# Kernel optimization log

Measured on AMD Instinct MI355X. Metric: run time of the kernel, lower is better.

Reference implementation:

```python
import jax, jax.numpy as jnp
import numpy as np
import math

N_NODES = 2000
LOOKBACK = 24
IN_DIM = 16
EMB_DIM = 64
BATCH = 32
LN_EPS = 1e-5


def _layernorm(v, g, b):
    mu = jnp.mean(v, axis=-1, keepdims=True)
    var = jnp.var(v, axis=-1, keepdims=True)
    return (v - mu) * jax.lax.rsqrt(var + LN_EPS) * g + b


def setup_inputs() -> dict:
    key = jax.random.key(0)
    ks = jax.random.split(key, 12)
    td = LOOKBACK * IN_DIM  # 384
    s_in = 1.0 / math.sqrt(td)
    s_d = 1.0 / math.sqrt(IN_DIM)
    return {
        "x": jax.random.normal(ks[0], (BATCH, N_NODES, LOOKBACK, IN_DIM), jnp.float32),
        "Wq": jax.random.normal(ks[1], (td, EMB_DIM), jnp.float32) * s_in,
        "bq": jax.random.normal(ks[2], (EMB_DIM,), jnp.float32) * 0.01,
        "Wk": jax.random.normal(ks[3], (td, EMB_DIM), jnp.float32) * s_in,
        "bk": jax.random.normal(ks[4], (EMB_DIM,), jnp.float32) * 0.01,
        "g0": jnp.ones((EMB_DIM,), jnp.float32),
        "beta0": jnp.zeros((EMB_DIM,), jnp.float32),
        "g1": jnp.ones((EMB_DIM,), jnp.float32),
        "beta1": jnp.zeros((EMB_DIM,), jnp.float32),
        "normal": jax.random.normal(ks[5], (N_NODES, LOOKBACK, IN_DIM), jnp.float32),
        "Win": jax.random.normal(ks[6], (IN_DIM, IN_DIM), jnp.float32) * s_d,
    }


def reference(x, Wq, bq, Wk, bk, g0, beta0, g1, beta1, normal, Win):
    b, n, t, d = x.shape
    xf = x.reshape(b, n, t * d)
    # per-sample q/k linear + layernorm (batched over b)
    q1 = _layernorm(xf @ Wq + bq, g0, beta0)  # (b, n, e)
    k1 = _layernorm(xf @ Wk + bk, g1, beta1)  # (b, n, e)
    # node-mixing attention: softmax(q k^T / sqrt(num_nodes)) @ normal
    scores = jnp.einsum('bne,bme->bnm', q1, k1) / math.sqrt(n)
    A = jax.nn.softmax(scores, axis=-1)  # (b, n, n)
    data = jnp.einsum('bnm,mf->bnf', A, normal.reshape(n, t * d)).reshape(b, n, t, d)
    # RPPsAtt attention weights over time (general attention, output_len = 1)
    query = x[:, :, -1, :] @ Win  # (b, n, d)
    att = jnp.einsum('bnd,bntd->bnt', query, data)  # scores vs context
    weight = jax.nn.softmax(att, axis=-1)  # (b, n, t)
    # res = stack(weights).permute(0,1,3,2) -> (b, n, t, 1), broadcast-add
    return data + weight[..., None]
```

## Files before the change

### kernel.cpp

```cpp
#include <hip/hip_runtime.h>
#include <math.h>

#define B_   32
#define NN   2000
#define NP   2048
#define TT   24
#define TD   384
#define EE   64
#define SCALE 0.022360679774997896f

typedef __bf16 bf16;
typedef __bf16 bf16x8 __attribute__((ext_vector_type(8)));
typedef float  f32x4  __attribute__((ext_vector_type(4)));

typedef __attribute__((address_space(3))) unsigned int       lds_u32;
typedef const __attribute__((address_space(1))) unsigned int g_u32;

__device__ __forceinline__ void dma16(const void* g, void* l) {
    __builtin_amdgcn_global_load_lds((g_u32*)g, (lds_u32*)l, 16, 0, 0);
}

__device__ __forceinline__ bool input_is_bf16(const void* g0) {
    return *reinterpret_cast<const unsigned short*>(g0) == 0x3F80;
}

__device__ __forceinline__ float safexp(float v) {
    return __expf(fminf(fmaxf(v, -30.f), 30.f));
}

__device__ __forceinline__ bf16x8 ld_frag(const bf16* p) {
    return *reinterpret_cast<const bf16x8*>(p);
}

__device__ __forceinline__ bf16x8 cvt8_f32(const float* p) {
    f32x4 a = *reinterpret_cast<const f32x4*>(p);
    f32x4 b = *reinterpret_cast<const f32x4*>(p + 4);
    bf16x8 r;
    r[0]=(bf16)a[0]; r[1]=(bf16)a[1]; r[2]=(bf16)a[2]; r[3]=(bf16)a[3];
    r[4]=(bf16)b[0]; r[5]=(bf16)b[1]; r[6]=(bf16)b[2]; r[7]=(bf16)b[3];
    return r;
}

__global__ void pack_w_k(const void* Wqv, const void* Wkv, bf16* __restrict__ Wp,
                         const void* gflag) {
    bool bf = input_is_bf16(gflag);
    int o = blockIdx.x * 256 + threadIdx.x;
    if (o >= 12*8*64*8) return;
    int j  = o & 7;
    int l  = (o >> 3) & 63;
    int nt = (o >> 9) & 7;
    int ks = o >> 12;
    int k   = ks*32 + ((l >> 4) * 8) + j;
    int col = nt*16 + (l & 15);
    float v;
    if (bf) v = (col < 64) ? (float)((const bf16*)Wqv)[k*64 + col]
                           : (float)((const bf16*)Wkv)[k*64 + col - 64];
    else    v = (col < 64) ? ((const float*)Wqv)[k*64 + col]
                           : ((const float*)Wkv)[k*64 + col - 64];
    Wp[o] = (bf16)v;
}

__global__ void pack_v_k(const void* normalv, bf16* __restrict__ Vp, const void* gflag) {
    bool bf = input_is_bf16(gflag);
    int o = blockIdx.x * 256 + threadIdx.x;
    if (o >= 64*25*512) return;
    int j  = o & 7;
    int l  = (o >> 3) & 63;
    int nt = (o >> 9) % 25;
    int kb = o / (25*512);
    int key = kb*32 + ((l >> 4) * 8) + j;
    int col = nt*16 + (l & 15);
    float v = 0.f;
    if (key < NN) {
        if (col < TD) v = bf ? (float)((const bf16*)normalv)[key*TD + col]
                             : ((const float*)normalv)[key*TD + col];
        else if (col == TD) v = 1.0f;
    }
    Vp[o] = (bf16)v;
}

__global__ void calc_query_k(const void* xv, const void* Winv, float* __restrict__ Qry,
                             const void* gflag) {
    bool bf = input_is_bf16(gflag);
    int o = blockIdx.x * 256 + threadIdx.x;
    if (o >= B_*NP*16) return;
    int d2 = o & 15;
    int n  = (o >> 4) & (NP - 1);
    int b  = o >> 15;
    float acc = 0.f;
    if (n < NN) {
        size_t xoff = ((size_t)(b*NN + n))*TD + (TT-1)*16;
        if (bf) {
            const bf16* xr = (const bf16*)xv + xoff;
            const bf16* Wn = (const bf16*)Winv;
            #pragma unroll
            for (int d = 0; d < 16; ++d) acc += (float)xr[d] * (float)Wn[d*16 + d2];
        } else {
            const float* xr = (const float*)xv + xoff;
            const float* Wn = (const float*)Winv;
            #pragma unroll
            for (int d = 0; d < 16; ++d) acc += xr[d] * Wn[d*16 + d2];
        }
    }
    Qry[o] = acc;
}

__global__ __launch_bounds__(256) void proj_ln_k(
        const void* xv, const bf16* __restrict__ Wp,
        const void* bqv, const void* bkv,
        const void* g0v, const void* be0v,
        const void* g1v, const void* be1v,
        bf16* __restrict__ Qb, bf16* __restrict__ Kp) {
    __shared__ __align__(16) bf16 Wbuf[2][4096];
    bool bf = input_is_bf16(g0v);
    int mb = blockIdx.x, b = blockIdx.y;
    int w    = threadIdx.x >> 6;
    int lane = threadIdx.x & 63;
    int quad = lane >> 4, lq = lane & 15;

    int rowA = mb*64 + w*16 + lq;
    int xrow = rowA < NN ? rowA : NN - 1;

    bf16x8 afr[12];
    if (bf) {
        const bf16* xp = (const bf16*)xv + ((size_t)(b*NN + xrow))*TD + quad*8;
        #pragma unroll
        for (int ks = 0; ks < 12; ++ks) afr[ks] = ld_frag(xp + ks*32);
    } else {
        const float* xp = (const float*)xv + ((size_t)(b*NN + xrow))*TD + quad*8;
        #pragma unroll
        for (int ks = 0; ks < 12; ++ks) afr[ks] = cvt8_f32(xp + ks*32);
    }

    auto stage = [&](int ks, int bufi) {
        const char* g = (const char*)Wp + (size_t)ks*8192;
        for (int c = w; c < 8; c += 4)
            dma16(g + c*1024 + (size_t)lane*16, &Wbuf[bufi][c*512]);
    };
    stage(0, 0);

    f32x4 acc[8];
    #pragma unroll
    for (int nt = 0; nt < 8; ++nt) acc[nt] = (f32x4){0.f, 0.f, 0.f, 0.f};
    __syncthreads();

    for (int ks = 0; ks < 12; ++ks) {
        int cur = ks & 1;
        if (ks + 1 < 12) stage(ks + 1, cur ^ 1);
        const bf16* wb = Wbuf[cur];
        #pragma unroll
        for (int nt = 0; nt < 8; ++nt) {
            bf16x8 bfr = ld_frag(wb + nt*512 + lane*8);
            acc[nt] = __builtin_amdgcn_mfma_f32_16x16x32_bf16(afr[ks], bfr, acc[nt], 0, 0, 0);
        }
        __syncthreads();
    }

    #pragma unroll
    for (int nt = 0; nt < 8; ++nt) {
        int c = nt*16 + lq;
        float bias;
        if (bf) bias = (c < 64) ? (float)((const bf16*)bqv)[c] : (float)((const bf16*)bkv)[c-64];
        else    bias = (c < 64) ? ((const float*)bqv)[c] : ((const float*)bkv)[c-64];
        #pragma unroll
        for (int r = 0; r < 4; ++r) acc[nt][r] += bias;
    }
    float outn[8][4];
    #pragma unroll
    for (int g = 0; g < 2; ++g) {
        float s[4], sq[4];
        #pragma unroll
        for (int r = 0; r < 4; ++r) {
            float p = 0.f, p2 = 0.f;
            #pragma unroll
            for (int nt = 0; nt < 4; ++nt) {
                float v = acc[g*4 + nt][r];
                p += v; p2 += v*v;
            }
            s[r] = p; sq[r] = p2;
        }
        #pragma unroll
        for (int m = 1; m < 16; m <<= 1) {
            #pragma unroll
            for (int r = 0; r < 4; ++r) {
                s[r]  += __shfl_xor(s[r],  m, 16);
                sq[r] += __shfl_xor(sq[r], m, 16);
            }
        }
        #pragma unroll
        for (int r = 0; r < 4; ++r) {
            float mean = s[r] * (1.f/64.f);
            float var  = fmaxf(sq[r] * (1.f/64.f) - mean*mean, 0.f);
            float rs   = rsqrtf(var + 1e-5f);
            #pragma unroll
            for (int nt = 0; nt < 4; ++nt) {
                int c = nt*16 + lq;
                float gv, bv;
                if (g == 0) { gv = bf ? (float)((const bf16*)g0v)[c] : ((const float*)g0v)[c];
                              bv = bf ? (float)((const bf16*)be0v)[c] : ((const float*)be0v)[c]; }
                else        { gv = bf ? (float)((const bf16*)g1v)[c] : ((const float*)g1v)[c];
                              bv = bf ? (float)((const bf16*)be1v)[c] : ((const float*)be1v)[c]; }
                outn[g*4 + nt][r] = (acc[g*4 + nt][r] - mean) * rs * gv + bv;
            }
        }
    }
    int rowq = mb*64 + w*16 + quad*4;
    #pragma unroll
    for (int r = 0; r < 4; ++r) {
        int row = rowq + r;
        bool real = row < NN;
        size_t qbase = ((size_t)(b*NP + row))*EE;
        int kb2  = row >> 5;
        int half = (row >> 4) & 1;
        int lqk  = row & 15;
        #pragma unroll
        for (int nt = 0; nt < 4; ++nt) {
            Qb[qbase + nt*16 + lq] = (bf16)(real ? outn[nt][r] : 0.f);
            int col   = nt*16 + lq;
            int f     = half*2 + (col >> 5);
            int quadk = (col >> 3) & 3;
            size_t idx = (((size_t)(b*64 + kb2)*4 + f)*64 + quadk*16 + lqk)*8 + (col & 7);
            Kp[idx] = (bf16)(real ? outn[4 + nt][r] : 0.f);
        }
    }
}

__global__ __launch_bounds__(512, 2) void attn_k(
        const bf16* __restrict__ Qb, const bf16* __restrict__ Kp,
        const bf16* __restrict__ Vp, const float* __restrict__ Qry,
        void* outv, const void* gflag) {
    __shared__ __align__(16) bf16 Kbuf[2][2048];
    __shared__ __align__(16) bf16 Vbuf[2][12800];
    __shared__ __align__(16) bf16 Pl[8][16][40];
    bool bf = input_is_bf16(gflag);
    int mb = blockIdx.x, b = blockIdx.y;
    int w    = threadIdx.x >> 6;
    int lane = threadIdx.x & 63;
    int quad = lane >> 4, lq = lane & 15;
    int rowbase = mb*128 + w*16;

    const bf16* qp = Qb + ((size_t)(b*NP + rowbase + lq))*EE + quad*8;
    bf16x8 aq0 = ld_frag(qp);
    bf16x8 aq1 = ld_frag(qp + 32);

    f32x4 acc[25];
    #pragma unroll
    for (int nt = 0; nt < 25; ++nt) acc[nt] = (f32x4){0.f, 0.f, 0.f, 0.f};

    const bf16* kg = Kp + (size_t)(b*64)*2048;
    auto stage = [&](int kb, int bufi) {
        const char* kgb = (const char*)(kg + (size_t)kb*2048);
        const char* vgb = (const char*)(Vp + (size_t)kb*12800);
        for (int c = w; c < 29; c += 8) {
            if (c < 4) dma16(kgb + c*1024 + (size_t)lane*16, &Kbuf[bufi][c*512]);
            else       dma16(vgb + (size_t)(c-4)*1024 + (size_t)lane*16, &Vbuf[bufi][(c-4)*512]);
        }
    };
    stage(0, 0);
    __syncthreads();

    for (int kb = 0; kb < 64; ++kb) {
        int cur = kb & 1;
        if (kb + 1 < 64) stage(kb + 1, cur ^ 1);
        const bf16* kc = Kbuf[cur];
        bf16x8 bk0 = ld_frag(kc + lane*8);
        bf16x8 bk1 = ld_frag(kc +  512 + lane*8);
        bf16x8 bk2 = ld_frag(kc + 1024 + lane*8);
        bf16x8 bk3 = ld_frag(kc + 1536 + lane*8);
        f32x4 s0 = (f32x4){0.f,0.f,0.f,0.f}, s1 = (f32x4){0.f,0.f,0.f,0.f};
        s0 = __builtin_amdgcn_mfma_f32_16x16x32_bf16(aq0, bk0, s0, 0, 0, 0);
        s0 = __builtin_amdgcn_mfma_f32_16x16x32_bf16(aq1, bk1, s0, 0, 0, 0);
        s1 = __builtin_amdgcn_mfma_f32_16x16x32_bf16(aq0, bk2, s1, 0, 0, 0);
        s1 = __builtin_amdgcn_mfma_f32_16x16x32_bf16(aq1, bk3, s1, 0, 0, 0);
        #pragma unroll
        for (int r = 0; r < 4; ++r) {
            Pl[w][quad*4 + r][lq]      = (bf16)safexp(s0[r] * SCALE);
            Pl[w][quad*4 + r][16 + lq] = (bf16)safexp(s1[r] * SCALE);
        }
        bf16x8 ap = ld_frag(&Pl[w][lq][quad*8]);
        const bf16* vc = Vbuf[cur];
        #pragma unroll
        for (int nt = 0; nt < 25; ++nt) {
            bf16x8 bv = ld_frag(vc + nt*512 + lane*8);
            acc[nt] = __builtin_amdgcn_mfma_f32_16x16x32_bf16(ap, bv, acc[nt], 0, 0, 0);
        }
        __syncthreads();
    }

    float inv[4];
    #pragma unroll
    for (int r = 0; r < 4; ++r) {
        float den = __shfl(acc[24][r], (lane & 48), 64);
        inv[r] = 1.f / fmaxf(den, 1e-30f);
    }
    #pragma unroll
    for (int nt = 0; nt < 24; ++nt)
        #pragma unroll
        for (int r = 0; r < 4; ++r) acc[nt][r] *= inv[r];

    float qd[4];
    #pragma unroll
    for (int r = 0; r < 4; ++r)
        qd[r] = Qry[(size_t)(b*NP + rowbase + quad*4 + r)*16 + lq];

    float dn[4] = {0.f, 0.f, 0.f, 0.f};
    #pragma unroll
    for (int t = 0; t < 24; ++t) {
        #pragma unroll
        for (int r = 0; r < 4; ++r) {
            float a = acc[t][r] * qd[r];
            a += __shfl_xor(a, 1, 16); a += __shfl_xor(a, 2, 16);
            a += __shfl_xor(a, 4, 16); a += __shfl_xor(a, 8, 16);
            dn[r] += safexp(a);
        }
    }
    #pragma unroll
    for (int r = 0; r < 4; ++r) dn[r] = 1.f / fmaxf(dn[r], 1e-30f);

    if (bf) {
        #pragma unroll
        for (int half = 0; half < 2; ++half) {
            __syncthreads();
            if ((w >> 2) == half && rowbase < NN) {
                bf16* scr = &Vbuf[0][0] + (w & 3)*6144;
                #pragma unroll
                for (int t = 0; t < 24; ++t) {
                    #pragma unroll
                    for (int r = 0; r < 4; ++r) {
                        float a = acc[t][r] * qd[r];
                        a += __shfl_xor(a, 1, 16); a += __shfl_xor(a, 2, 16);
                        a += __shfl_xor(a, 4, 16); a += __shfl_xor(a, 8, 16);
                        float wv = safexp(a) * dn[r];
                        scr[(quad*4 + r)*384 + t*16 + lq] = (bf16)(acc[t][r] + wv);
                    }
                }
                bf16* og = (bf16*)outv + ((size_t)b*NN + rowbase)*TD;
                #pragma unroll
                for (int i = 0; i < 12; ++i)
                    *reinterpret_cast<bf16x8*>(og + i*512 + lane*8) =
                        *reinterpret_cast<const bf16x8*>(scr + i*512 + lane*8);
            }
        }
    } else {
        #pragma unroll
        for (int t = 0; t < 24; ++t) {
            #pragma unroll
            for (int r = 0; r < 4; ++r) {
                float a = acc[t][r] * qd[r];
                a += __shfl_xor(a, 1, 16); a += __shfl_xor(a, 2, 16);
                a += __shfl_xor(a, 4, 16); a += __shfl_xor(a, 8, 16);
                float wv = safexp(a) * dn[r];
                int row = rowbase + quad*4 + r;
                if (row < NN)
                    ((float*)outv)[((size_t)(b*NN + row))*TD + t*16 + lq] = acc[t][r] + wv;
            }
        }
    }
}

extern "C" void kernel_launch(void* const* d_in, const int* in_sizes, int n_in,
                              void* d_out, int out_size, void* d_ws, size_t ws_size,
                              hipStream_t stream) {
    const void* x      = d_in[0];
    const void* Wq     = d_in[1];
    const void* bq     = d_in[2];
    const void* Wk     = d_in[3];
    const void* bk     = d_in[4];
    const void* g0     = d_in[5];
    const void* be0    = d_in[6];
    const void* g1     = d_in[7];
    const void* be1    = d_in[8];
    const void* normal = d_in[9];
    const void* Win    = d_in[10];

    char* ws = (char*)d_ws;
    bf16*  Qb  = (bf16*)(ws);
    bf16*  Kp  = (bf16*)(ws + 8388608);
    bf16*  Vp  = (bf16*)(ws + 16777216);
    bf16*  Wp  = (bf16*)(ws + 16777216 + 1638400);
    float* Qry = (float*)(ws + 16777216 + 1638400 + 98304);

    pack_w_k<<<dim3(192), dim3(256), 0, stream>>>(Wq, Wk, Wp, g0);
    pack_v_k<<<dim3(3200), dim3(256), 0, stream>>>(normal, Vp, g0);
    calc_query_k<<<dim3(4096), dim3(256), 0, stream>>>(x, Win, Qry, g0);
    proj_ln_k<<<dim3(32, 32), dim3(256), 0, stream>>>(x, Wp, bq, bk, g0, be0, g1, be1, Qb, Kp);
    attn_k<<<dim3(16, 32), dim3(512), 0, stream>>>(Qb, Kp, Vp, Qry, d_out, g0);
}
```

Before: 423.5 us.

## Split PV accumulation across waves by output column tiles with shared P

The attention kernel now has each wave compute the softmax probabilities for its own 16 query rows and write them into shared LDS. Every wave then multiplies all 128 rows by only 3 of the 24 value column tiles, instead of all 25 tiles for its own 16 rows. This drops the ones-column denominator tile in favour of a register-side row sum with masking, and skips the final all-padding key block. The time-softmax reduction goes through an LDS exchange buffer. The aim is to cut redundant V fragment loads per wave and the extra MFMA tile, at the cost of an extra barrier per key block and more LDS traffic for P and the epilogue.

New measurement: 412.1 us. -2.7%, faster.

```diff
diff --git a/kernel.cpp b/kernel.cpp
--- a/kernel.cpp
+++ b/kernel.cpp
@@ -63,19 +63,17 @@
 __global__ void pack_v_k(const void* normalv, bf16* __restrict__ Vp, const void* gflag) {
     bool bf = input_is_bf16(gflag);
     int o = blockIdx.x * 256 + threadIdx.x;
-    if (o >= 64*25*512) return;
+    if (o >= 64*24*512) return;
     int j  = o & 7;
     int l  = (o >> 3) & 63;
-    int nt = (o >> 9) % 25;
-    int kb = o / (25*512);
+    int nt = (o >> 9) % 24;
+    int kb = o / (24*512);
     int key = kb*32 + ((l >> 4) * 8) + j;
     int col = nt*16 + (l & 15);
     float v = 0.f;
-    if (key < NN) {
-        if (col < TD) v = bf ? (float)((const bf16*)normalv)[key*TD + col]
-                             : ((const float*)normalv)[key*TD + col];
-        else if (col == TD) v = 1.0f;
-    }
+    if (key < NN)
+        v = bf ? (float)((const bf16*)normalv)[key*TD + col]
+               : ((const float*)normalv)[key*TD + col];
     Vp[o] = (bf16)v;
 }
 
@@ -229,40 +227,52 @@
         const bf16* __restrict__ Qb, const bf16* __restrict__ Kp,
         const bf16* __restrict__ Vp, const float* __restrict__ Qry,
         void* outv, const void* gflag) {
-    __shared__ __align__(16) bf16 Kbuf[2][2048];
-    __shared__ __align__(16) bf16 Vbuf[2][12800];
-    __shared__ __align__(16) bf16 Pl[8][16][40];
+    __shared__ __align__(16) char SM[66560];
+    bf16*  Kb    = (bf16*)(SM);
+    bf16*  Vb    = (bf16*)(SM + 8192);
+    bf16*  Pl    = (bf16*)(SM + 57344);
+    bf16*  scr   = (bf16*)(SM);
+    float* eBuf  = (float*)(SM + 52224);
+    float* invD  = (float*)(SM + 65536);
+    float* dnInv = (float*)(SM + 66048);
+
     bool bf = input_is_bf16(gflag);
     int mb = blockIdx.x, b = blockIdx.y;
     int w    = threadIdx.x >> 6;
     int lane = threadIdx.x & 63;
     int quad = lane >> 4, lq = lane & 15;
-    int rowbase = mb*128 + w*16;
-
-    const bf16* qp = Qb + ((size_t)(b*NP + rowbase + lq))*EE + quad*8;
+    int rowbase = mb*128;
+    int myrow16 = rowbase + w*16;
+
+    const bf16* qp = Qb + ((size_t)(b*NP + myrow16 + lq))*EE + quad*8;
     bf16x8 aq0 = ld_frag(qp);
     bf16x8 aq1 = ld_frag(qp + 32);
 
-    f32x4 acc[25];
-    #pragma unroll
-    for (int nt = 0; nt < 25; ++nt) acc[nt] = (f32x4){0.f, 0.f, 0.f, 0.f};
+    f32x4 acc[8][3];
+    #pragma unroll
+    for (int rt = 0; rt < 8; ++rt)
+        #pragma unroll
+        for (int ct = 0; ct < 3; ++ct) acc[rt][ct] = (f32x4){0.f, 0.f, 0.f, 0.f};
+    float den[4] = {0.f, 0.f, 0.f, 0.f};
 
     const bf16* kg = Kp + (size_t)(b*64)*2048;
     auto stage = [&](int kb, int bufi) {
         const char* kgb = (const char*)(kg + (size_t)kb*2048);
-        const char* vgb = (const char*)(Vp + (size_t)kb*12800);
-        for (int c = w; c < 29; c += 8) {
-            if (c < 4) dma16(kgb + c*1024 + (size_t)lane*16, &Kbuf[bufi][c*512]);
-            else       dma16(vgb + (size_t)(c-4)*1024 + (size_t)lane*16, &Vbuf[bufi][(c-4)*512]);
+        const char* vgb = (const char*)(Vp + (size_t)kb*12288);
+        for (int c = w; c < 28; c += 8) {
+            if (c < 4) dma16(kgb + c*1024 + (size_t)lane*16, Kb + bufi*2048 + c*512);
+            else       dma16(vgb + (size_t)(c-4)*1024 + (size_t)lane*16,
+                             Vb + bufi*12288 + (c-4)*512);
         }
     };
     stage(0, 0);
     __syncthreads();
 
-    for (int kb = 0; kb < 64; ++kb) {
+    for (int kb = 0; kb < 63; ++kb) {
         int cur = kb & 1;
-        if (kb + 1 < 64) stage(kb + 1, cur ^ 1);
-        const bf16* kc = Kbuf[cur];
+        if (kb + 1 < 63) stage(kb + 1, cur ^ 1);
+
+        const bf16* kc = Kb + cur*2048;
         bf16x8 bk0 = ld_frag(kc + lane*8);
         bf16x8 bk1 = ld_frag(kc +  512 + lane*8);
         bf16x8 bk2 = ld_frag(kc + 1024 + lane*8);
@@ -272,87 +282,133 @@
         s0 = __builtin_amdgcn_mfma_f32_16x16x32_bf16(aq1, bk1, s0, 0, 0, 0);
         s1 = __builtin_amdgcn_mfma_f32_16x16x32_bf16(aq0, bk2, s1, 0, 0, 0);
         s1 = __builtin_amdgcn_mfma_f32_16x16x32_bf16(aq1, bk3, s1, 0, 0, 0);
+
+        int k0ok = (kb*32 + lq)      < NN;
+        int k1ok = (kb*32 + 16 + lq) < NN;
+        bf16* pw = Pl + w*512;
+        int pb = (lq >> 3)*128 + quad*32 + (lq & 7);
         #pragma unroll
         for (int r = 0; r < 4; ++r) {
-            Pl[w][quad*4 + r][lq]      = (bf16)safexp(s0[r] * SCALE);
-            Pl[w][quad*4 + r][16 + lq] = (bf16)safexp(s1[r] * SCALE);
-        }
-        bf16x8 ap = ld_frag(&Pl[w][lq][quad*8]);
-        const bf16* vc = Vbuf[cur];
-        #pragma unroll
-        for (int nt = 0; nt < 25; ++nt) {
-            bf16x8 bv = ld_frag(vc + nt*512 + lane*8);
-            acc[nt] = __builtin_amdgcn_mfma_f32_16x16x32_bf16(ap, bv, acc[nt], 0, 0, 0);
+            float e0 = safexp(s0[r] * SCALE);
+            float e1 = safexp(s1[r] * SCALE);
+            den[r] += (k0ok ? e0 : 0.f) + (k1ok ? e1 : 0.f);
+            pw[pb + r*8]       = (bf16)e0;
+            pw[pb + 256 + r*8] = (bf16)e1;
+        }
+
+        const bf16* vc = Vb + cur*12288;
+        bf16x8 bv0 = ld_frag(vc + (w*3 + 0)*512 + lane*8);
+        bf16x8 bv1 = ld_frag(vc + (w*3 + 1)*512 + lane*8);
+        bf16x8 bv2 = ld_frag(vc + (w*3 + 2)*512 + lane*8);
+
+        asm volatile("s_waitcnt lgkmcnt(0)" ::: "memory");
+        __builtin_amdgcn_s_barrier();
+        asm volatile("" ::: "memory");
+        __builtin_amdgcn_sched_barrier(0);
+
+        #pragma unroll
+        for (int rt = 0; rt < 8; ++rt) {
+            bf16x8 ap = ld_frag(Pl + rt*512 + lane*8);
+            acc[rt][0] = __builtin_amdgcn_mfma_f32_16x16x32_bf16(ap, bv0, acc[rt][0], 0, 0, 0);
+            acc[rt][1] = __builtin_amdgcn_mfma_f32_16x16x32_bf16(ap, bv1, acc[rt][1], 0, 0, 0);
+            acc[rt][2] = __builtin_amdgcn_mfma_f32_16x16x32_bf16(ap, bv2, acc[rt][2], 0, 0, 0);
         }
         __syncthreads();
     }
 
-    float inv[4];
     #pragma unroll
     for (int r = 0; r < 4; ++r) {
-        float den = __shfl(acc[24][r], (lane & 48), 64);
-        inv[r] = 1.f / fmaxf(den, 1e-30f);
-    }
-    #pragma unroll
-    for (int nt = 0; nt < 24; ++nt)
-        #pragma unroll
-        for (int r = 0; r < 4; ++r) acc[nt][r] *= inv[r];
-
-    float qd[4];
-    #pragma unroll
-    for (int r = 0; r < 4; ++r)
-        qd[r] = Qry[(size_t)(b*NP + rowbase + quad*4 + r)*16 + lq];
-
-    float dn[4] = {0.f, 0.f, 0.f, 0.f};
-    #pragma unroll
-    for (int t = 0; t < 24; ++t) {
+        float s = den[r];
+        s += __shfl_xor(s, 1, 16); s += __shfl_xor(s, 2, 16);
+        s += __shfl_xor(s, 4, 16); s += __shfl_xor(s, 8, 16);
+        den[r] = 1.f / fmaxf(s, 1e-30f);
+    }
+    if (lq == 0) {
+        #pragma unroll
+        for (int r = 0; r < 4; ++r) invD[w*16 + quad*4 + r] = den[r];
+    }
+    __syncthreads();
+
+    const float* qryb = Qry + ((size_t)(b*NP + rowbase))*16 + lq;
+    #pragma unroll
+    for (int rt = 0; rt < 8; ++rt) {
+        float inv[4], qd[4];
         #pragma unroll
         for (int r = 0; r < 4; ++r) {
-            float a = acc[t][r] * qd[r];
-            a += __shfl_xor(a, 1, 16); a += __shfl_xor(a, 2, 16);
-            a += __shfl_xor(a, 4, 16); a += __shfl_xor(a, 8, 16);
-            dn[r] += safexp(a);
-        }
-    }
-    #pragma unroll
-    for (int r = 0; r < 4; ++r) dn[r] = 1.f / fmaxf(dn[r], 1e-30f);
+            inv[r] = invD[rt*16 + quad*4 + r];
+            qd[r]  = qryb[(size_t)(rt*16 + quad*4 + r)*16];
+        }
+        #pragma unroll
+        for (int ct = 0; ct < 3; ++ct) {
+            #pragma unroll
+            for (int r = 0; r < 4; ++r) {
+                float v = acc[rt][ct][r] * inv[r];
+                acc[rt][ct][r] = v;
+                float a = v * qd[r];
+                a += __shfl_xor(a, 1, 16); a += __shfl_xor(a, 2, 16);
+                a += __shfl_xor(a, 4, 16); a += __shfl_xor(a, 8, 16);
+                float e = safexp(a);
+                if (lq == 0) eBuf[(rt*16 + quad*4 + r)*26 + (w*3 + ct)] = e;
+            }
+        }
+    }
+    __syncthreads();
+
+    if (lane < 16) {
+        int row = w*16 + lane;
+        float s = 0.f;
+        #pragma unroll
+        for (int t = 0; t < 24; ++t) s += eBuf[row*26 + t];
+        dnInv[row] = 1.f / fmaxf(s, 1e-30f);
+    }
+    __syncthreads();
 
     if (bf) {
         #pragma unroll
         for (int half = 0; half < 2; ++half) {
-            __syncthreads();
-            if ((w >> 2) == half && rowbase < NN) {
-                bf16* scr = &Vbuf[0][0] + (w & 3)*6144;
+            #pragma unroll
+            for (int rti = 0; rti < 4; ++rti) {
+                int rt = half*4 + rti;
                 #pragma unroll
-                for (int t = 0; t < 24; ++t) {
+                for (int ct = 0; ct < 3; ++ct) {
+                    int t = w*3 + ct;
                     #pragma unroll
                     for (int r = 0; r < 4; ++r) {
-                        float a = acc[t][r] * qd[r];
-                        a += __shfl_xor(a, 1, 16); a += __shfl_xor(a, 2, 16);
-                        a += __shfl_xor(a, 4, 16); a += __shfl_xor(a, 8, 16);
-                        float wv = safexp(a) * dn[r];
-                        scr[(quad*4 + r)*384 + t*16 + lq] = (bf16)(acc[t][r] + wv);
+                        int row = rt*16 + quad*4 + r;
+                        float wv = eBuf[row*26 + t] * dnInv[row];
+                        float outv_ = (half ? acc[4 + rti][ct][r] : acc[rti][ct][r]) + wv;
+                        scr[(size_t)(row - half*64)*408 + t*16 + lq] = (bf16)outv_;
                     }
                 }
-                bf16* og = (bf16*)outv + ((size_t)b*NN + rowbase)*TD;
+            }
+            __syncthreads();
+            bf16* og = (bf16*)outv + ((size_t)b*NN + rowbase + half*64)*TD;
+            #pragma unroll
+            for (int i = 0; i < 8; ++i) {
+                int lrow = w*8 + i;
+                int grow = rowbase + half*64 + lrow;
+                if (grow < NN && lane < 48)
+                    *reinterpret_cast<bf16x8*>(og + (size_t)lrow*TD + lane*8) =
+                        *reinterpret_cast<const bf16x8*>(scr + (size_t)lrow*408 + lane*8);
+            }
+            __syncthreads();
+        }
+    } else {
+        #pragma unroll
+        for (int rt = 0; rt < 8; ++rt) {
+            #pragma unroll
+            for (int ct = 0; ct < 3; ++ct) {
+                int t = w*3 + ct;
                 #pragma unroll
-                for (int i = 0; i < 12; ++i)
-                    *reinterpret_cast<bf16x8*>(og + i*512 + lane*8) =
-                        *reinterpret_cast<const bf16x8*>(scr + i*512 + lane*8);
-            }
-        }
-    } else {
-        #pragma unroll
-        for (int t = 0; t < 24; ++t) {
-            #pragma unroll
-            for (int r = 0; r < 4; ++r) {
-                float a = acc[t][r] * qd[r];
-                a += __shfl_xor(a, 1, 16); a += __shfl_xor(a, 2, 16);
-                a += __shfl_xor(a, 4, 16); a += __shfl_xor(a, 8, 16);
-                float wv = safexp(a) * dn[r];
-                int row = rowbase + quad*4 + r;
-                if (row < NN)
-                    ((float*)outv)[((size_t)(b*NN + row))*TD + t*16 + lq] = acc[t][r] + wv;
+                for (int r = 0; r < 4; ++r) {
+                    int row  = rt*16 + quad*4 + r;
+                    int grow = rowbase + row;
+                    if (grow < NN) {
+                        float wv = eBuf[row*26 + t] * dnInv[row];
+                        ((float*)outv)[((size_t)(b*NN + grow))*TD + t*16 + lq] =
+                            acc[rt][ct][r] + wv;
+                    }
+                }
             }
         }
     }
@@ -381,7 +437,7 @@
     float* Qry = (float*)(ws + 16777216 + 1638400 + 98304);
 
     pack_w_k<<<dim3(192), dim3(256), 0, stream>>>(Wq, Wk, Wp, g0);
-    pack_v_k<<<dim3(3200), dim3(256), 0, stream>>>(normal, Vp, g0);
+    pack_v_k<<<dim3(3072), dim3(256), 0, stream>>>(normal, Vp, g0);
     calc_query_k<<<dim3(4096), dim3(256), 0, stream>>>(x, Win, Qry, g0);
     proj_ln_k<<<dim3(32, 32), dim3(256), 0, stream>>>(x, Wp, bq, bk, g0, be0, g1, be1, Qb, Kp);
     attn_k<<<dim3(16, 32), dim3(512), 0, stream>>>(Qb, Kp, Vp, Qry, d_out, g0);
```
